# Kernel optimization log

Hardware: AMD Instinct MI355X
Metric: run time of the kernel (lower is better)

## Reference

```python
import jax, jax.numpy as jnp
import numpy as np

# ---- static module config (matches torch defaults) ----
N_LEVELS = 16
MIN_RES = 16
MAX_RES = 512
N_ENC = 2 ** 14
D = 3          # n_input_dims
E = 2          # n_embed_dims
B = 1 << 20    # number of query points

# per-level resolutions, computed in float32 to mirror torch's float32 log/exp
_gf = np.exp((np.log(np.float32(MAX_RES)) - np.log(np.float32(MIN_RES))) / np.float32(N_LEVELS - 1)).astype(np.float32)
RES = [int(np.floor(np.float32(MIN_RES) * _gf ** np.float32(l))) for l in range(N_LEVELS)]
DIRECT = [r ** D < N_ENC for r in RES]                  # small grids use direct ravel indexing
NLE = [min(r ** D, N_ENC) for r in RES]                  # encodings per level (sentinel row at index NLE[l])

# 2^D corner offsets, shape (8, 3)
OFFS = np.stack(np.meshgrid(*([np.arange(2)] * D), indexing='ij'), axis=-1).reshape(-1, D).astype(np.int32)
# instant-ngp spatial hashing primes
PRIMES = (1, 2654435761, 805459861)


def setup_inputs() -> dict:
    key = jax.random.key(0)
    k1, k2 = jax.random.split(key)
    x = jax.random.uniform(k1, (B, D), dtype=jnp.float32, minval=-1.0, maxval=1.0)
    # stacked per-level tables, padded to (N_ENC+1, E); rows >= NLE[l] zeroed
    emb = jax.random.uniform(k2, (N_LEVELS, N_ENC + 1, E), dtype=jnp.float32, minval=-1e-4, maxval=1e-4)
    row = np.arange(N_ENC + 1)
    valid = (row[None, :] < np.asarray(NLE)[:, None])    # (L, N_ENC+1); also zeroes the sentinel row
    emb = emb * jnp.asarray(valid[..., None], dtype=jnp.float32)
    return {"x": x, "emb": emb}


def _level_features(x, emb_l, R, n_encs, direct):
    offs = jnp.asarray(OFFS)                             # (8, 3)
    xs = (x + 1.0) * (R * 0.5) - 0.5                     # grid coords
    xl = jnp.floor(xs)
    frac = xs - xl                                       # (B, 3)
    xi = xl.astype(jnp.int32)
    c = xi[:, None, :] + offs[None, :, :]                # (B, 8, 3) corner indices
    # bilinear/trilinear weights: prod over dims of frac (offset=1) or 1-frac (offset=0)
    w = jnp.prod(jnp.where(offs[None].astype(bool), frac[:, None, :], 1.0 - frac[:, None, :]), axis=-1)  # (B, 8)
    w = jax.lax.stop_gradient(w)                         # torch computes weights under no_grad
    m = jnp.all((c >= 0) & (c < R), axis=-1)             # (B, 8) corner validity
    if direct:
        ids = (c[..., 0] * R + c[..., 1]) * R + c[..., 2]
    else:
        cu = c.astype(jnp.uint32)
        h = (cu[..., 0] * jnp.uint32(PRIMES[0])
             ^ cu[..., 1] * jnp.uint32(PRIMES[1])
             ^ cu[..., 2] * jnp.uint32(PRIMES[2]))
        ids = (h % jnp.uint32(n_encs)).astype(jnp.int32)
    ids = jnp.where(m, ids, n_encs)                      # invalid corners -> zero sentinel row
    return jnp.sum(emb_l[ids] * w[..., None], axis=1)    # (B, E)


def reference(x, emb):
    feats = [
        _level_features(x, emb[l], RES[l], NLE[l], DIRECT[l])
        for l in range(N_LEVELS)
    ]
    return jnp.stack(feats, axis=1)                      # (B, L, E)
```

## Files before the change

### kernel.cpp

```cpp
#include <hip/hip_runtime.h>


typedef __attribute__((ext_vector_type(2))) float f32x2;

#define B_POINTS (1 << 20)
#define N_LEVELS 16
#define TAB_F2   16385
#define WG       1024
#define NWG      256
#define NCHUNK   (NWG / N_LEVELS)
#define CHUNK    (B_POINTS / NCHUNK)
#define PPT      (CHUNK / WG)
#define GRP      4
#define NGRP     (PPT / GRP)

__constant__ int   cRES[N_LEVELS]  = {16, 20, 25, 32, 40, 50, 64, 80,
                                      101, 128, 161, 203, 256, 322, 406, 512};
__constant__ float cHALF[N_LEVELS] = {8.f, 10.f, 12.5f, 16.f, 20.f, 25.f, 32.f, 40.f,
                                      50.5f, 64.f, 80.5f, 101.5f, 128.f, 161.f, 203.f, 256.f};

__global__ __launch_bounds__(WG)
void hashenc_lds(const float* __restrict__ x,
                 const float* __restrict__ emb,
                 float* __restrict__ out)
{
    __shared__ f32x2 tab[TAB_F2];

    const int bid = blockIdx.x;
    const int xcd = bid & 7;
    const int s   = bid >> 3;
    const int l   = s & 15;
    const int c   = ((s >> 4) << 3) | xcd;

    const int   R      = cRES[l];
    const int   Rm1    = R - 1;
    const float half   = cHALF[l];
    const float hb     = half - 0.5f;
    const bool  direct = (l < 3);
    const int   R8     = R * 8;
    const int   RR8    = R * R * 8;

    const f32x2* __restrict__ gtab = (const f32x2*)emb + (size_t)l * TAB_F2;
    const int t    = threadIdx.x;
    const int base = c * CHUNK + t;

    float xa[GRP], xb[GRP], xcv[GRP];
#pragma unroll
    for (int j = 0; j < GRP; ++j) {
        const int p = base + j * WG;
        xa[j] = x[p * 3 + 0]; xb[j] = x[p * 3 + 1]; xcv[j] = x[p * 3 + 2];
    }

#pragma unroll
    for (int j = 0; j < 16; ++j)
        tab[j * WG + t] = gtab[j * WG + t];
    if (t == 0) tab[16384] = gtab[16384];
    __syncthreads();

    const char* tb = (const char*)tab;

    for (int kg = 0; kg < NGRP; ++kg) {
        float ca[GRP], cb[GRP], cc[GRP];
#pragma unroll
        for (int j = 0; j < GRP; ++j) { ca[j] = xa[j]; cb[j] = xb[j]; cc[j] = xcv[j]; }

        if (kg + 1 < NGRP) {
#pragma unroll
            for (int j = 0; j < GRP; ++j) {
                const int p = base + (kg + 1) * (GRP * WG) + j * WG;
                xa[j] = x[p * 3 + 0]; xb[j] = x[p * 3 + 1]; xcv[j] = x[p * 3 + 2];
            }
        }

#pragma unroll
        for (int j = 0; j < GRP; ++j) {
            const int p = base + kg * (GRP * WG) + j * WG;

            const float xs0 = fmaf(ca[j], half, hb);
            const float xs1 = fmaf(cb[j], half, hb);
            const float xs2 = fmaf(cc[j], half, hb);
            const float fl0 = floorf(xs0), fl1 = floorf(xs1), fl2 = floorf(xs2);
            const float f0 = xs0 - fl0, f1 = xs1 - fl1, f2 = xs2 - fl2;
            const float g0 = 1.0f - f0, g1 = 1.0f - f1, g2 = 1.0f - f2;
            const int i0 = (int)fl0, i1 = (int)fl1, i2 = (int)fl2;

            const float wx0 = (i0 >= 0)  ? g0 : 0.0f;
            const float wx1 = (i0 < Rm1) ? f0 : 0.0f;
            const float wy0 = (i1 >= 0)  ? g1 : 0.0f;
            const float wy1 = (i1 < Rm1) ? f1 : 0.0f;
            const float wz0 = (i2 >= 0)  ? g2 : 0.0f;
            const float wz1 = (i2 < Rm1) ? f2 : 0.0f;

            const float pxy00 = wx0 * wy0, pxy01 = wx0 * wy1;
            const float pxy10 = wx1 * wy0, pxy11 = wx1 * wy1;
            const float w0 = pxy00 * wz0, w1 = pxy00 * wz1;
            const float w2 = pxy01 * wz0, w3 = pxy01 * wz1;
            const float w4 = pxy10 * wz0, w5 = pxy10 * wz1;
            const float w6 = pxy11 * wz0, w7 = pxy11 * wz1;

            unsigned d0, d1, d2, d3, d4, d5, d6, d7;
            if (direct) {
                const int u0l = max(i0, 0), u0h = min(i0 + 1, Rm1);
                const int u1l = max(i1, 0), u1h = min(i1 + 1, Rm1);
                const int u2l = max(i2, 0), u2h = min(i2 + 1, Rm1);
                const int a0  = u0l * RR8,     a1  = u0h * RR8;
                const int b00 = a0 + u1l * R8, b01 = a0 + u1h * R8;
                const int b10 = a1 + u1l * R8, b11 = a1 + u1h * R8;
                const int zl  = u2l * 8,       zh  = u2h * 8;
                d0 = b00 + zl; d1 = b00 + zh; d2 = b01 + zl; d3 = b01 + zh;
                d4 = b10 + zl; d5 = b10 + zh; d6 = b11 + zl; d7 = b11 + zh;
            } else {
                const unsigned MB  = 16383u << 3;
                const unsigned hx0 = (unsigned)i0 << 3,                 hx1 = hx0 + 8u;
                const unsigned hy0 = (unsigned)i1 * (2654435761u * 8u), hy1 = hy0 + (2654435761u * 8u);
                const unsigned hzf = (unsigned)i2 * (805459861u * 8u);
                const unsigned hz0 = hzf & MB, hz1 = (hzf + (805459861u * 8u)) & MB;
                const unsigned t00 = (hx0 ^ hy0) & MB, t01 = (hx0 ^ hy1) & MB;
                const unsigned t10 = (hx1 ^ hy0) & MB, t11 = (hx1 ^ hy1) & MB;
                d0 = t00 ^ hz0; d1 = t00 ^ hz1; d2 = t01 ^ hz0; d3 = t01 ^ hz1;
                d4 = t10 ^ hz0; d5 = t10 ^ hz1; d6 = t11 ^ hz0; d7 = t11 ^ hz1;
            }

            f32x2 acc = *(const f32x2*)(tb + d0) * w0;
            acc += *(const f32x2*)(tb + d1) * w1;
            acc += *(const f32x2*)(tb + d2) * w2;
            acc += *(const f32x2*)(tb + d3) * w3;
            acc += *(const f32x2*)(tb + d4) * w4;
            acc += *(const f32x2*)(tb + d5) * w5;
            acc += *(const f32x2*)(tb + d6) * w6;
            acc += *(const f32x2*)(tb + d7) * w7;

            ((f32x2*)out)[(size_t)p * N_LEVELS + l] = acc;
        }
    }
}

extern "C" void kernel_launch(void* const* d_in, const int* in_sizes, int n_in,
                              void* d_out, int out_size, void* d_ws, size_t ws_size,
                              hipStream_t stream) {
    const float* x   = (const float*)d_in[0];
    const float* emb = (const float*)d_in[1];
    float* out = (float*)d_out;

    hashenc_lds<<<NWG, WG, 0, stream>>>(x, emb, out);
}
```

Measured before the change: 211.7 us.

## Store per-level embedding tables in LDS as fp16 and double workgroup count

Converts each level's embedding table to half2 when staging it into shared memory, halving its LDS footprint to 64KB. This allows more resident workgroups per CU, so the grid is doubled to 512 blocks with a launch-bounds occupancy hint. Gathers read half2 and accumulate in fp32. The cost is a precision loss on the table values (fp16 rounding of values around 1e-4, near the subnormal range). The sentinel row copy is dropped, which is safe only because clamped or masked corners never index it.

```diff
diff --git a/kernel.cpp b/kernel.cpp
--- a/kernel.cpp
+++ b/kernel.cpp
@@ -1,4 +1,5 @@
 #include <hip/hip_runtime.h>
+#include <hip/hip_fp16.h>
 
 
 typedef __attribute__((ext_vector_type(2))) float f32x2;
@@ -6,8 +7,9 @@
 #define B_POINTS (1 << 20)
 #define N_LEVELS 16
 #define TAB_F2   16385
+#define TAB_H2   16384
 #define WG       1024
-#define NWG      256
+#define NWG      512
 #define NCHUNK   (NWG / N_LEVELS)
 #define CHUNK    (B_POINTS / NCHUNK)
 #define PPT      (CHUNK / WG)
@@ -19,12 +21,12 @@
 __constant__ float cHALF[N_LEVELS] = {8.f, 10.f, 12.5f, 16.f, 20.f, 25.f, 32.f, 40.f,
                                       50.5f, 64.f, 80.5f, 101.5f, 128.f, 161.f, 203.f, 256.f};
 
-__global__ __launch_bounds__(WG)
+__global__ __launch_bounds__(WG, 8)
 void hashenc_lds(const float* __restrict__ x,
                  const float* __restrict__ emb,
                  float* __restrict__ out)
 {
-    __shared__ f32x2 tab[TAB_F2];
+    __shared__ __half2 tab[TAB_H2];
 
     const int bid = blockIdx.x;
     const int xcd = bid & 7;
@@ -37,8 +39,8 @@
     const float half   = cHALF[l];
     const float hb     = half - 0.5f;
     const bool  direct = (l < 3);
-    const int   R8     = R * 8;
-    const int   RR8    = R * R * 8;
+    const int   R4     = R * 4;
+    const int   RR4    = R * R * 4;
 
     const f32x2* __restrict__ gtab = (const f32x2*)emb + (size_t)l * TAB_F2;
     const int t    = threadIdx.x;
@@ -52,9 +54,13 @@
     }
 
 #pragma unroll
-    for (int j = 0; j < 16; ++j)
-        tab[j * WG + t] = gtab[j * WG + t];
-    if (t == 0) tab[16384] = gtab[16384];
+    for (int j = 0; j < 16; ++j) {
+        const f32x2 v = gtab[j * WG + t];
+        __half2 h;
+        h.x = __float2half_rn(v.x);
+        h.y = __float2half_rn(v.y);
+        tab[j * WG + t] = h;
+    }
     __syncthreads();
 
     const char* tb = (const char*)tab;
@@ -103,34 +109,45 @@
                 const int u0l = max(i0, 0), u0h = min(i0 + 1, Rm1);
                 const int u1l = max(i1, 0), u1h = min(i1 + 1, Rm1);
                 const int u2l = max(i2, 0), u2h = min(i2 + 1, Rm1);
-                const int a0  = u0l * RR8,     a1  = u0h * RR8;
-                const int b00 = a0 + u1l * R8, b01 = a0 + u1h * R8;
-                const int b10 = a1 + u1l * R8, b11 = a1 + u1h * R8;
-                const int zl  = u2l * 8,       zh  = u2h * 8;
+                const int a0  = u0l * RR4,     a1  = u0h * RR4;
+                const int b00 = a0 + u1l * R4, b01 = a0 + u1h * R4;
+                const int b10 = a1 + u1l * R4, b11 = a1 + u1h * R4;
+                const int zl  = u2l * 4,       zh  = u2h * 4;
                 d0 = b00 + zl; d1 = b00 + zh; d2 = b01 + zl; d3 = b01 + zh;
                 d4 = b10 + zl; d5 = b10 + zh; d6 = b11 + zl; d7 = b11 + zh;
             } else {
-                const unsigned MB  = 16383u << 3;
-                const unsigned hx0 = (unsigned)i0 << 3,                 hx1 = hx0 + 8u;
-                const unsigned hy0 = (unsigned)i1 * (2654435761u * 8u), hy1 = hy0 + (2654435761u * 8u);
-                const unsigned hzf = (unsigned)i2 * (805459861u * 8u);
-                const unsigned hz0 = hzf & MB, hz1 = (hzf + (805459861u * 8u)) & MB;
+                const unsigned MB  = 16383u << 2;
+                const unsigned hx0 = (unsigned)i0 << 2,                 hx1 = hx0 + 4u;
+                const unsigned hy0 = (unsigned)i1 * (2654435761u * 4u), hy1 = hy0 + (2654435761u * 4u);
+                const unsigned hzf = (unsigned)i2 * (805459861u * 4u);
+                const unsigned hz0 = hzf & MB, hz1 = (hzf + (805459861u * 4u)) & MB;
                 const unsigned t00 = (hx0 ^ hy0) & MB, t01 = (hx0 ^ hy1) & MB;
                 const unsigned t10 = (hx1 ^ hy0) & MB, t11 = (hx1 ^ hy1) & MB;
                 d0 = t00 ^ hz0; d1 = t00 ^ hz1; d2 = t01 ^ hz0; d3 = t01 ^ hz1;
                 d4 = t10 ^ hz0; d5 = t10 ^ hz1; d6 = t11 ^ hz0; d7 = t11 ^ hz1;
             }
 
-            f32x2 acc = *(const f32x2*)(tb + d0) * w0;
-            acc += *(const f32x2*)(tb + d1) * w1;
-            acc += *(const f32x2*)(tb + d2) * w2;
-            acc += *(const f32x2*)(tb + d3) * w3;
-            acc += *(const f32x2*)(tb + d4) * w4;
-            acc += *(const f32x2*)(tb + d5) * w5;
-            acc += *(const f32x2*)(tb + d6) * w6;
-            acc += *(const f32x2*)(tb + d7) * w7;
+            float acc0 = 0.0f, acc1 = 0.0f;
+            {
+                const __half2 e0 = *(const __half2*)(tb + d0);
+                const __half2 e1 = *(const __half2*)(tb + d1);
+                const __half2 e2 = *(const __half2*)(tb + d2);
+                const __half2 e3 = *(const __half2*)(tb + d3);
+                const __half2 e4 = *(const __half2*)(tb + d4);
+                const __half2 e5 = *(const __half2*)(tb + d5);
+                const __half2 e6 = *(const __half2*)(tb + d6);
+                const __half2 e7 = *(const __half2*)(tb + d7);
+                acc0 = fmaf(__low2float(e0),  w0, acc0); acc1 = fmaf(__high2float(e0), w0, acc1);
+                acc0 = fmaf(__low2float(e1),  w1, acc0); acc1 = fmaf(__high2float(e1), w1, acc1);
+                acc0 = fmaf(__low2float(e2),  w2, acc0); acc1 = fmaf(__high2float(e2), w2, acc1);
+                acc0 = fmaf(__low2float(e3),  w3, acc0); acc1 = fmaf(__high2float(e3), w3, acc1);
+                acc0 = fmaf(__low2float(e4),  w4, acc0); acc1 = fmaf(__high2float(e4), w4, acc1);
+                acc0 = fmaf(__low2float(e5),  w5, acc0); acc1 = fmaf(__high2float(e5), w5, acc1);
+                acc0 = fmaf(__low2float(e6),  w6, acc0); acc1 = fmaf(__high2float(e6), w6, acc1);
+                acc0 = fmaf(__low2float(e7),  w7, acc0); acc1 = fmaf(__high2float(e7), w7, acc1);
+            }
 
-            ((f32x2*)out)[(size_t)p * N_LEVELS + l] = acc;
+            ((float2*)out)[(size_t)p * N_LEVELS + l] = make_float2(acc0, acc1);
         }
     }
 }
```

Result: no change. 209.7 us (-1.0%).
